# Optimization experiments

Measured on AMD Instinct MI355X. Metric: run time of the kernel, lower is better.

Reference implementation:

```python
import jax, jax.numpy as jnp
import numpy as np

B, S, D, F, H = 64, 1024, 512, 256, 512


def setup_inputs() -> dict:
    key = jax.random.key(0)
    ks = jax.random.split(key, 13)
    sd = lambda fan_in: 1.0 / np.sqrt(fan_in)
    return {
        "x": jax.random.normal(ks[0], (B, D), jnp.float32),
        "encoder_outputs": jax.random.normal(ks[1], (B, S, D), jnp.float32),
        "field_embeddings": jax.random.normal(ks[2], (B, S, F), jnp.float32),
        # Dense params: field_embs_TIL (F->H), enc_outs_TIL (D->H),
        # state_fields_L (D->H), state_enc_outs_L (D->H), out_gate_L (2D->H)
        "W_f": jax.random.normal(ks[3], (F, H), jnp.float32) * sd(F),
        "b_f": jnp.zeros((H,), jnp.float32),
        "W_e": jax.random.normal(ks[4], (D, H), jnp.float32) * sd(D),
        "b_e": jnp.zeros((H,), jnp.float32),
        "W_sf": jax.random.normal(ks[5], (D, H), jnp.float32) * sd(D),
        "b_sf": jnp.zeros((H,), jnp.float32),
        "W_se": jax.random.normal(ks[6], (D, H), jnp.float32) * sd(D),
        "b_se": jnp.zeros((H,), jnp.float32),
        "W_g": jax.random.normal(ks[7], (2 * D, H), jnp.float32) * sd(2 * D),
        "b_g": jnp.zeros((H,), jnp.float32),
    }


def reference(x, encoder_outputs, field_embeddings,
              W_f, b_f, W_e, b_e, W_sf, b_sf, W_se, b_se, W_g, b_g):
    # calc_timestep_consts: seq-major layout [S, B, feat]
    enc_outs = jnp.transpose(encoder_outputs, (1, 0, 2))        # [S,B,D]
    fields = jnp.transpose(field_embeddings, (1, 0, 2))          # [S,B,F]
    fe_TI = jnp.tanh(fields @ W_f + b_f)                         # [S,B,H]
    eo_TI = jnp.tanh(enc_outs @ W_e + b_e)                       # [S,B,H]

    # call(x)
    state_tanh_f = jnp.tanh(x @ W_sf + b_sf)                     # [B,H]
    state_tanh_x = jnp.tanh(x @ W_se + b_se)                     # [B,H]

    score_enc_outs = jnp.einsum('bh,sbh->sb', state_tanh_x, eo_TI)  # [S,B]
    score_fields = jnp.einsum('bh,sbh->sb', state_tanh_f, fe_TI)    # [S,B]
    alphas = jax.nn.softmax(score_enc_outs, axis=0)
    betas = jax.nn.softmax(score_fields, axis=0)

    ab = alphas * betas
    gammas = ab / (1e-6 + jnp.sum(ab, axis=0, keepdims=True))    # [S,B]

    context = jnp.einsum('sb,sbd->bd', gammas, enc_outs)          # [B,D]
    out = jnp.tanh(jnp.concatenate([context, x], axis=-1) @ W_g + b_g)  # [B,H]
    return out, gammas
```

## Files before the change

kernel.cpp:

```cpp
#include <hip/hip_runtime.h>

#define B_ 64
#define S_ 1024
#define D_ 512
#define F_ 256
#define H_ 512

#define FLAGS_W  0
#define ST_F_W   16
#define ST_X_W   32784
#define SC_E_W   65552
#define SC_F_W   131088
#define WPEL_W   196624
#define WPFL_W   327696
#define CTX_W    393232
#define WPEH_W   426000
#define WPFH_W   557072
#define CANARY_W 622608

typedef __attribute__((ext_vector_type(8))) short bf16x8;
typedef __attribute__((ext_vector_type(4))) short bf16x4;
typedef __attribute__((ext_vector_type(4))) float f32x4;
typedef unsigned short u16;
typedef unsigned int u32;

__device__ inline float bf2f(u16 u) {
  u32 i = ((u32)u) << 16;
  float f;
  __builtin_memcpy(&f, &i, 4);
  return f;
}
__device__ inline u16 f2bf(float f) {
  u32 i;
  __builtin_memcpy(&i, &f, 4);
  u32 r = i + 0x7fffu + ((i >> 16) & 1u);
  return (u16)(r >> 16);
}
__device__ inline void split_bf(float v, u16& h, u16& l) {
  u32 i;
  __builtin_memcpy(&i, &v, 4);
  h = (u16)(i >> 16);
  u32 hb = i & 0xFFFF0000u;
  float hf;
  __builtin_memcpy(&hf, &hb, 4);
  l = f2bf(v - hf);
}
__device__ inline u32 cvt_pk_bf16(float a, float b) {
  u32 r;
  asm("v_cvt_pk_bf16_f32 %0, %1, %2" : "=v"(r) : "v"(a), "v"(b));
  return r;
}
__device__ inline float ldin(const void* p, size_t i, int f32) {
  return f32 ? ((const float*)p)[i] : bf2f(((const u16*)p)[i]);
}
__device__ inline void stout(void* p, size_t i, float v, int f32) {
  if (f32) ((float*)p)[i] = v;
  else ((u16*)p)[i] = f2bf(v);
}
__device__ inline float fast_tanh(float x) {
  float cx = fminf(15.f, fmaxf(-15.f, x));
  float e = __expf(2.f * cx);
  return (e - 1.f) * __builtin_amdgcn_rcpf(e + 1.f);
}

__global__ void prep_kernel(const u16* __restrict__ We16,
                            const void* __restrict__ We, const void* __restrict__ Wf,
                            const void* __restrict__ x,
                            const void* __restrict__ Wsf, const void* __restrict__ bsf,
                            const void* __restrict__ Wse, const void* __restrict__ bse,
                            float* __restrict__ st_f, float* __restrict__ st_x,
                            u16* __restrict__ WpEH, u16* __restrict__ WpEL,
                            u16* __restrict__ WpFH, u16* __restrict__ WpFL,
                            u32* __restrict__ flags, u32* __restrict__ canary,
                            float* __restrict__ ctx) {
  __shared__ u32 cnt;
  if (threadIdx.x == 0) cnt = 0;
  __syncthreads();
  u32 local = 0;
  for (int i = threadIdx.x; i < 1024; i += 256) {
    u32 e = (We16[i] >> 7) & 0xFF;
    if (e >= 134) ++local;
  }
  if (local) atomicAdd(&cnt, local);
  __syncthreads();
  const int f32 = cnt > 64;
  const int bid = blockIdx.x, t = threadIdx.x;

  if (bid < 32) {
    int i = bid * 1024 + t * 4;
    *(f32x4*)&ctx[i] = (f32x4){0.f, 0.f, 0.f, 0.f};
    if (bid == 0 && t == 0) {
      flags[0] = (u32)f32;
      for (int i2 = 1; i2 < 16; ++i2) flags[i2] = 0;
      canary[0] = 0xC0DE0001u; canary[1] = 0xC0DE0002u;
      canary[2] = 0xC0DE0003u; canary[3] = 0xC0DE0004u;
    }
    return;
  }
  if (bid < 288) {
    int tid = (bid - 32) * 256 + t;
    int h = tid & 511, b = (tid >> 9) & 63, which = tid >> 15;
    const void* W = which ? Wse : Wsf;
    const void* bias = which ? bse : bsf;
    float a[8] = {};
    for (int d = 0; d < D_; d += 8) {
#pragma unroll
      for (int j = 0; j < 8; ++j)
        a[j] += ldin(x, b * D_ + d + j, f32) * ldin(W, (size_t)(d + j) * H_ + h, f32);
    }
    float acc = ((a[0] + a[1]) + (a[2] + a[3])) + ((a[4] + a[5]) + (a[6] + a[7]));
    float v = fast_tanh(acc + ldin(bias, h, f32));
    (which ? st_x : st_f)[b * H_ + h] = v;
    return;
  }
  int tb = bid - 288;
  const void* W;
  u16 *WpH, *WpL;
  int K;
  if (tb < 128) { W = We; WpH = WpEH; WpL = WpEL; K = 512; }
  else          { W = Wf; WpH = WpFH; WpL = WpFL; K = 256; tb -= 128; }
  int tg = tb * 256 + t;
  int lane = tg & 63, tile = tg >> 6;
  int kc = tile >> 5, nc = tile & 31;
  int kb = kc * 32 + ((lane >> 4) << 3);
  int nb = nc * 16 + (lane & 15);
  u16 vh[8], vl[8];
#pragma unroll
  for (int j = 0; j < 8; ++j) {
    float v = ldin(W, (size_t)(kb + j) * H_ + nb, f32);
    split_bf(v, vh[j], vl[j]);
  }
  size_t off = ((size_t)tile << 9) + (size_t)lane * 8;
#pragma unroll
  for (int j = 0; j < 8; ++j) {
    WpH[off + j] = vh[j];
    WpL[off + j] = vl[j];
  }
}

__global__ void __launch_bounds__(512, 2) score2_kernel(
    const void* __restrict__ enc, const void* __restrict__ fld,
    const u16* __restrict__ WpEH, const u16* __restrict__ WpEL,
    const u16* __restrict__ WpFH, const u16* __restrict__ WpFL,
    const void* __restrict__ be, const void* __restrict__ bfp,
    const float* __restrict__ stx, const float* __restrict__ stf,
    float* __restrict__ sce, float* __restrict__ scf,
    const u32* __restrict__ flags) {
  constexpr int KP = 128, LDK = KP + 8;
  __shared__ __attribute__((aligned(16))) short AsH[2][64 * LDK];
  __shared__ __attribute__((aligned(16))) short AsL[2][64 * LDK];
  __shared__ float scw[8][64];
  const int f32 = flags[0];
  const int tid = threadIdx.x;
  int bid = blockIdx.x;
  const int sel = bid >> 10;
  bid &= 1023;
  const void* A    = sel ? fld : enc;
  const u16* WpH   = sel ? WpFH : WpEH;
  const u16* WpL   = sel ? WpFL : WpEL;
  const void* bias = sel ? bfp : be;
  const float* st  = sel ? stf : stx;
  float* score     = sel ? scf : sce;
  const int K = sel ? F_ : D_;
  const int NPH = K >> 7, NK = NPH * 4;

  const int m0 = bid * 64;
  const int b = m0 >> 10, s0 = m0 & 1023;
  const int lane = tid & 63, wave = tid >> 6;
  const int ml = lane & 15, q = lane >> 4;
  const int nb = wave * 4;
  const bf16x8* wph = (const bf16x8*)WpH;
  const bf16x8* wpl = (const bf16x8*)WpL;
  const int sr = tid >> 5, scc = tid & 31;
  f32x4 pre[4];
  bf16x4 preb[4];

#define ISSUE_LOADS(PH)                                                              \
  do {                                                                               \
    if (f32) {                                                                       \
      _Pragma("unroll") for (int it = 0; it < 4; ++it)                               \
          pre[it] = *(const f32x4*)((const float*)A +                                \
                                    (size_t)(m0 + sr + 16 * it) * K + (PH)*KP + scc * 4); \
    } else {                                                                         \
      _Pragma("unroll") for (int it = 0; it < 4; ++it)                               \
          preb[it] = *(const bf16x4*)((const u16*)A +                                \
                                      (size_t)(m0 + sr + 16 * it) * K + (PH)*KP + scc * 4); \
    }                                                                                \
  } while (0)

#define WRITE_STAGE(BUF)                                                             \
  do {                                                                               \
    _Pragma("unroll") for (int it = 0; it < 4; ++it) {                               \
      u32 iv[4];                                                                     \
      float vf[4];                                                                   \
      if (f32) {                                                                     \
        _Pragma("unroll") for (int j = 0; j < 4; ++j) {                              \
          vf[j] = pre[it][j];                                                        \
          __builtin_memcpy(&iv[j], &vf[j], 4);                                       \
        }                                                                            \
      } else {                                                                       \
        _Pragma("unroll") for (int j = 0; j < 4; ++j) {                              \
          iv[j] = ((u32)(u16)preb[it][j]) << 16;                                     \
          __builtin_memcpy(&vf[j], &iv[j], 4);                                       \
        }                                                                            \
      }                                                                              \
      u32 h01 = __builtin_amdgcn_perm(iv[1], iv[0], 0x07060302u);                    \
      u32 h23 = __builtin_amdgcn_perm(iv[3], iv[2], 0x07060302u);                    \
      float hf[4];                                                                   \
      _Pragma("unroll") for (int j = 0; j < 4; ++j) {                                \
        u32 hb = iv[j] & 0xFFFF0000u;                                                \
        __builtin_memcpy(&hf[j], &hb, 4);                                            \
      }                                                                              \
      u32 l01 = cvt_pk_bf16(vf[0] - hf[0], vf[1] - hf[1]);                           \
      u32 l23 = cvt_pk_bf16(vf[2] - hf[2], vf[3] - hf[3]);                           \
      u32* dH = (u32*)&AsH[BUF][(sr + 16 * it) * LDK + scc * 4];                     \
      u32* dL = (u32*)&AsL[BUF][(sr + 16 * it) * LDK + scc * 4];                     \
      dH[0] = h01; dH[1] = h23;                                                      \
      dL[0] = l01; dL[1] = l23;                                                      \
    }                                                                                \
  } while (0)

#define LOAD_B(DH, DL, KCG)                                                          \
  do {                                                                               \
    _Pragma("unroll") for (int ns = 0; ns < 4; ++ns) {                               \
      size_t widx = (size_t)((KCG)*32 + nb + ns) * 64 + lane;                        \
      DH[ns] = wph[widx];                                                            \
      DL[ns] = wpl[widx];                                                            \
    }                                                                                \
  } while (0)

  f32x4 acc[4][4] = {};
  bf16x8 bh[4], bl[4], bhn[4], bln[4];
  ISSUE_LOADS(0);
  WRITE_STAGE(0);
  ISSUE_LOADS(1);
  LOAD_B(bh, bl, 0);
  __syncthreads();
  for (int ph = 0; ph < NPH; ++ph) {
    const int cur = ph & 1, nxt = cur ^ 1;
#pragma unroll
    for (int kc = 0; kc < 4; ++kc) {
      const int kcg = ph * 4 + kc;
      const int kcn = (kcg + 1 < NK) ? (kcg + 1) : kcg;
      LOAD_B(bhn, bln, kcn);
      bf16x8 ah[4], al[4];
#pragma unroll
      for (int ms = 0; ms < 4; ++ms) {
        ah[ms] = *(const bf16x8*)&AsH[cur][(ms * 16 + ml) * LDK + kc * 32 + q * 8];
        al[ms] = *(const bf16x8*)&AsL[cur][(ms * 16 + ml) * LDK + kc * 32 + q * 8];
      }
      if (kc == 2 && ph + 1 < NPH) WRITE_STAGE(nxt);
      if (kc == 3 && ph + 2 < NPH) ISSUE_LOADS(ph + 2);
      __builtin_amdgcn_s_setprio(1);
#pragma unroll
      for (int ms = 0; ms < 4; ++ms)
#pragma unroll
        for (int ns = 0; ns < 4; ++ns) {
          acc[ms][ns] = __builtin_amdgcn_mfma_f32_16x16x32_bf16(ah[ms], bh[ns], acc[ms][ns], 0, 0, 0);
          acc[ms][ns] = __builtin_amdgcn_mfma_f32_16x16x32_bf16(al[ms], bh[ns], acc[ms][ns], 0, 0, 0);
          acc[ms][ns] = __builtin_amdgcn_mfma_f32_16x16x32_bf16(ah[ms], bl[ns], acc[ms][ns], 0, 0, 0);
        }
      __builtin_amdgcn_s_setprio(0);
#pragma unroll
      for (int ns = 0; ns < 4; ++ns) { bh[ns] = bhn[ns]; bl[ns] = bln[ns]; }
    }
    __syncthreads();
  }
  float biasn[4], stn[4];
#pragma unroll
  for (int ns = 0; ns < 4; ++ns) {
    int n = (nb + ns) * 16 + ml;
    biasn[ns] = ldin(bias, n, f32);
    stn[ns] = st[b * H_ + n];
  }
#pragma unroll
  for (int ms = 0; ms < 4; ++ms) {
#pragma unroll
    for (int r = 0; r < 4; ++r) {
      float p = 0.f;
#pragma unroll
      for (int ns = 0; ns < 4; ++ns)
        p += fast_tanh(acc[ms][ns][r] + biasn[ns]) * stn[ns];
      p += __shfl_xor(p, 1);
      p += __shfl_xor(p, 2);
      p += __shfl_xor(p, 4);
      p += __shfl_xor(p, 8);
      if (ml == 0) scw[wave][ms * 16 + q * 4 + r] = p;
    }
  }
  __syncthreads();
  if (tid < 64) {
    float s = 0.f;
#pragma unroll
    for (int w = 0; w < 8; ++w) s += scw[w][tid];
    score[b * S_ + s0 + tid] = s;
  }
#undef ISSUE_LOADS
#undef WRITE_STAGE
#undef LOAD_B
}

__device__ inline float block_reduce_max(float v, float* red, int tid) {
#pragma unroll
  for (int off = 32; off >= 1; off >>= 1) v = fmaxf(v, __shfl_xor(v, off));
  if ((tid & 63) == 0) red[tid >> 6] = v;
  __syncthreads();
  v = fmaxf(fmaxf(red[0], red[1]), fmaxf(red[2], red[3]));
  __syncthreads();
  return v;
}
__device__ inline float block_reduce_sum(float v, float* red, int tid) {
#pragma unroll
  for (int off = 32; off >= 1; off >>= 1) v += __shfl_xor(v, off);
  if ((tid & 63) == 0) red[tid >> 6] = v;
  __syncthreads();
  v = red[0] + red[1] + red[2] + red[3];
  __syncthreads();
  return v;
}

__global__ void ctx2_kernel(const float* __restrict__ se, const float* __restrict__ sf,
                            const void* __restrict__ enc, float* __restrict__ ctx,
                            void* __restrict__ dout, u32* __restrict__ flags) {
  __shared__ float red[4];
  __shared__ float gl[S_];
  const int f32 = flags[0];
  int b = blockIdx.x >> 4, sc = blockIdx.x & 15;
  int t = threadIdx.x;
  float e[4], f[4];
  int bad = 0;
#pragma unroll
  for (int i = 0; i < 4; ++i) {
    e[i] = se[b * S_ + t + 256 * i];
    f[i] = sf[b * S_ + t + 256 * i];
    if (!(fabsf(e[i]) < 1e4f) || !(fabsf(f[i]) < 1e4f)) bad = 1;
  }
  if (bad && sc == 0) flags[4] = 1;
  float me = block_reduce_max(fmaxf(fmaxf(e[0], e[1]), fmaxf(e[2], e[3])), red, t);
  float mf = block_reduce_max(fmaxf(fmaxf(f[0], f[1]), fmaxf(f[2], f[3])), red, t);
  float sume = 0.f, sumf = 0.f;
#pragma unroll
  for (int i = 0; i < 4; ++i) {
    e[i] = __expf(e[i] - me);
    sume += e[i];
    f[i] = __expf(f[i] - mf);
    sumf += f[i];
  }
  sume = block_reduce_sum(sume, red, t);
  sumf = block_reduce_sum(sumf, red, t);
  float g[4], tot = 0.f;
#pragma unroll
  for (int i = 0; i < 4; ++i) {
    g[i] = (e[i] / sume) * (f[i] / sumf);
    tot += g[i];
  }
  tot = block_reduce_sum(tot, red, t);
  float scale = 1.f / (1e-6f + tot);
#pragma unroll
  for (int i = 0; i < 4; ++i) {
    int s = t + 256 * i;
    float gv = g[i] * scale;
    gl[s] = gv;
    if (sc == 0) stout(dout, (size_t)B_ * H_ + (size_t)s * B_ + b, gv, f32);
  }
  __syncthreads();
  int d0 = t * 2;
  float a0 = 0.f, a1 = 0.f;
#pragma unroll 4
  for (int s = sc * 64; s < sc * 64 + 64; ++s) {
    float gv = gl[s];
    size_t base = ((size_t)(b * S_ + s)) * D_ + d0;
    a0 += gv * ldin(enc, base, f32);
    a1 += gv * ldin(enc, base + 1, f32);
  }
  atomicAdd(&ctx[b * D_ + d0], a0);
  atomicAdd(&ctx[b * D_ + d0 + 1], a1);
}

__global__ void out_kernel(const float* __restrict__ ctx, const void* __restrict__ x,
                           const void* __restrict__ Wg, const void* __restrict__ bg,
                           void* __restrict__ dout, const u32* __restrict__ flags,
                           const u32* __restrict__ canary) {
  const int f32 = flags[0];
  int tid = blockIdx.x * 256 + threadIdx.x;
  int h = tid & 511, b = tid >> 9;
  float a0 = 0.f, a1 = 0.f, a2 = 0.f, a3 = 0.f;
  for (int d = 0; d < D_; d += 4) {
    a0 += ctx[b * D_ + d]     * ldin(Wg, (size_t)d * H_ + h, f32);
    a1 += ctx[b * D_ + d + 1] * ldin(Wg, (size_t)(d + 1) * H_ + h, f32);
    a2 += ctx[b * D_ + d + 2] * ldin(Wg, (size_t)(d + 2) * H_ + h, f32);
    a3 += ctx[b * D_ + d + 3] * ldin(Wg, (size_t)(d + 3) * H_ + h, f32);
  }
  for (int d = 0; d < D_; d += 4) {
    a0 += ldin(x, b * D_ + d, f32)     * ldin(Wg, (size_t)(D_ + d) * H_ + h, f32);
    a1 += ldin(x, b * D_ + d + 1, f32) * ldin(Wg, (size_t)(D_ + d + 1) * H_ + h, f32);
    a2 += ldin(x, b * D_ + d + 2, f32) * ldin(Wg, (size_t)(D_ + d + 2) * H_ + h, f32);
    a3 += ldin(x, b * D_ + d + 3, f32) * ldin(Wg, (size_t)(D_ + d + 3) * H_ + h, f32);
  }
  float acc = (a0 + a1) + (a2 + a3);
  float v = fast_tanh(acc + ldin(bg, h, f32));
  if (tid == 0) {
    u32 code = 0;
    if (canary[0] != 0xC0DE0001u || canary[1] != 0xC0DE0002u ||
        canary[2] != 0xC0DE0003u || canary[3] != 0xC0DE0004u) code += 32;
    if (flags[4]) code += 64;
    if (code) v = (float)code;
  }
  stout(dout, (size_t)b * H_ + h, v, f32);
}

extern "C" void kernel_launch(void* const* d_in, const int* in_sizes, int n_in,
                              void* d_out, int out_size, void* d_ws, size_t ws_size,
                              hipStream_t stream) {
  const void* x    = d_in[0];
  const void* enc  = d_in[1];
  const void* fld  = d_in[2];
  const void* W_f  = d_in[3];
  const void* b_f  = d_in[4];
  const void* W_e  = d_in[5];
  const void* b_e  = d_in[6];
  const void* W_sf = d_in[7];
  const void* b_sf = d_in[8];
  const void* W_se = d_in[9];
  const void* b_se = d_in[10];
  const void* W_g  = d_in[11];
  const void* b_g  = d_in[12];

  float* ws    = (float*)d_ws;
  u32* flags   = (u32*)(ws + FLAGS_W);
  float* st_f  = ws + ST_F_W;
  float* st_x  = ws + ST_X_W;
  float* sc_e  = ws + SC_E_W;
  float* sc_f  = ws + SC_F_W;
  float* ctx   = ws + CTX_W;
  u16* WpEH    = (u16*)(ws + WPEH_W);
  u16* WpEL    = (u16*)(ws + WPEL_W);
  u16* WpFH    = (u16*)(ws + WPFH_W);
  u16* WpFL    = (u16*)(ws + WPFL_W);
  u32* canary  = (u32*)(ws + CANARY_W);

  prep_kernel<<<480, 256, 0, stream>>>((const u16*)W_e, W_e, W_f, x,
                                       W_sf, b_sf, W_se, b_se, st_f, st_x,
                                       WpEH, WpEL, WpFH, WpFL, flags, canary, ctx);
  score2_kernel<<<2048, 512, 0, stream>>>(enc, fld, WpEH, WpEL, WpFH, WpFL,
                                          b_e, b_f, st_x, st_f, sc_e, sc_f, flags);
  ctx2_kernel<<<1024, 256, 0, stream>>>(sc_e, sc_f, enc, ctx, d_out, flags);
  out_kernel<<<128, 256, 0, stream>>>(ctx, x, W_g, b_g, d_out, flags, canary);
}
```

Measured before the change: 560.7 us.

## Specialize score kernel on K and hoist dtype branches out of inner loops

Turns the score GEMM body into a template on K so the phase loop fully unrolls, and precomputes byte offsets for LDS and B-fragment addressing. It also double-buffers the B fragments by index instead of copying registers each step. In the prep, context and output kernels, the per-element ldin dtype switch is replaced by separate f32 and bf16 loops using pointer-increment addressing. The intent is less address arithmetic and branching in hot loops, at the cost of larger code and more register pressure.

```diff
diff --git a/kernel.cpp b/kernel.cpp
--- a/kernel.cpp
+++ b/kernel.cpp
@@ -21,6 +21,7 @@
 typedef __attribute__((ext_vector_type(8))) short bf16x8;
 typedef __attribute__((ext_vector_type(4))) short bf16x4;
 typedef __attribute__((ext_vector_type(4))) float f32x4;
+typedef __attribute__((ext_vector_type(2))) unsigned int u32x2;
 typedef unsigned short u16;
 typedef unsigned int u32;
 
@@ -100,15 +101,24 @@
   if (bid < 288) {
     int tid = (bid - 32) * 256 + t;
     int h = tid & 511, b = (tid >> 9) & 63, which = tid >> 15;
-    const void* W = which ? Wse : Wsf;
+    float a[8] = {};
+    if (f32) {
+      const float* xp = (const float*)x + b * D_;
+      const float* Wp = (const float*)(which ? Wse : Wsf) + h;
+      for (int d = 0; d < D_; d += 8)
+#pragma unroll
+        for (int j = 0; j < 8; ++j)
+          a[j] += xp[d + j] * Wp[(size_t)(d + j) * H_];
+    } else {
+      const u16* xp = (const u16*)x + b * D_;
+      const u16* Wp = (const u16*)(which ? Wse : Wsf) + h;
+      for (int d = 0; d < D_; d += 8)
+#pragma unroll
+        for (int j = 0; j < 8; ++j)
+          a[j] += bf2f(xp[d + j]) * bf2f(Wp[(size_t)(d + j) * H_]);
+    }
+    float acc = ((a[0] + a[1]) + (a[2] + a[3])) + ((a[4] + a[5]) + (a[6] + a[7]));
     const void* bias = which ? bse : bsf;
-    float a[8] = {};
-    for (int d = 0; d < D_; d += 8) {
-#pragma unroll
-      for (int j = 0; j < 8; ++j)
-        a[j] += ldin(x, b * D_ + d + j, f32) * ldin(W, (size_t)(d + j) * H_ + h, f32);
-    }
-    float acc = ((a[0] + a[1]) + (a[2] + a[3])) + ((a[4] + a[5]) + (a[6] + a[7]));
     float v = fast_tanh(acc + ldin(bias, h, f32));
     (which ? st_x : st_f)[b * H_ + h] = v;
     return;
@@ -116,20 +126,26 @@
   int tb = bid - 288;
   const void* W;
   u16 *WpH, *WpL;
-  int K;
-  if (tb < 128) { W = We; WpH = WpEH; WpL = WpEL; K = 512; }
-  else          { W = Wf; WpH = WpFH; WpL = WpFL; K = 256; tb -= 128; }
+  if (tb < 128) { W = We; WpH = WpEH; WpL = WpEL; }
+  else          { W = Wf; WpH = WpFH; WpL = WpFL; tb -= 128; }
   int tg = tb * 256 + t;
   int lane = tg & 63, tile = tg >> 6;
   int kc = tile >> 5, nc = tile & 31;
   int kb = kc * 32 + ((lane >> 4) << 3);
   int nb = nc * 16 + (lane & 15);
+  float v[8];
+  if (f32) {
+    const float* Wp = (const float*)W + (size_t)kb * H_ + nb;
+#pragma unroll
+    for (int j = 0; j < 8; ++j) v[j] = Wp[(size_t)j * H_];
+  } else {
+    const u16* Wp = (const u16*)W + (size_t)kb * H_ + nb;
+#pragma unroll
+    for (int j = 0; j < 8; ++j) v[j] = bf2f(Wp[(size_t)j * H_]);
+  }
   u16 vh[8], vl[8];
 #pragma unroll
-  for (int j = 0; j < 8; ++j) {
-    float v = ldin(W, (size_t)(kb + j) * H_ + nb, f32);
-    split_bf(v, vh[j], vl[j]);
-  }
+  for (int j = 0; j < 8; ++j) split_bf(v[j], vh[j], vl[j]);
   size_t off = ((size_t)tile << 9) + (size_t)lane * 8;
 #pragma unroll
   for (int j = 0; j < 8; ++j) {
@@ -138,40 +154,24 @@
   }
 }
 
-__global__ void __launch_bounds__(512, 2) score2_kernel(
-    const void* __restrict__ enc, const void* __restrict__ fld,
-    const u16* __restrict__ WpEH, const u16* __restrict__ WpEL,
-    const u16* __restrict__ WpFH, const u16* __restrict__ WpFL,
-    const void* __restrict__ be, const void* __restrict__ bfp,
-    const float* __restrict__ stx, const float* __restrict__ stf,
-    float* __restrict__ sce, float* __restrict__ scf,
-    const u32* __restrict__ flags) {
-  constexpr int KP = 128, LDK = KP + 8;
-  __shared__ __attribute__((aligned(16))) short AsH[2][64 * LDK];
-  __shared__ __attribute__((aligned(16))) short AsL[2][64 * LDK];
-  __shared__ float scw[8][64];
-  const int f32 = flags[0];
-  const int tid = threadIdx.x;
-  int bid = blockIdx.x;
-  const int sel = bid >> 10;
-  bid &= 1023;
-  const void* A    = sel ? fld : enc;
-  const u16* WpH   = sel ? WpFH : WpEH;
-  const u16* WpL   = sel ? WpFL : WpEL;
-  const void* bias = sel ? bfp : be;
-  const float* st  = sel ? stf : stx;
-  float* score     = sel ? scf : sce;
-  const int K = sel ? F_ : D_;
-  const int NPH = K >> 7, NK = NPH * 4;
+template <int K>
+__device__ __forceinline__ void score_core(
+    const void* __restrict__ A, const bf16x8* __restrict__ wph,
+    const bf16x8* __restrict__ wpl, const void* __restrict__ bias,
+    const float* __restrict__ st, float* __restrict__ score,
+    int f32, int bid, int tid, char* AsHb, char* AsLb, float (*scw)[64]) {
+  constexpr int KP = 128, LDK = KP + 8, NPH = K / KP, NK = NPH * 4;
+  constexpr int BUFB = 64 * LDK * 2;
 
   const int m0 = bid * 64;
   const int b = m0 >> 10, s0 = m0 & 1023;
   const int lane = tid & 63, wave = tid >> 6;
   const int ml = lane & 15, q = lane >> 4;
   const int nb = wave * 4;
-  const bf16x8* wph = (const bf16x8*)WpH;
-  const bf16x8* wpl = (const bf16x8*)WpL;
   const int sr = tid >> 5, scc = tid & 31;
+  const u32 bofsB = ((u32)(nb * 64 + lane)) * 16u;
+  const u32 aoffB = ((u32)(ml * LDK + q * 8)) * 2u;
+  const u32 woffB = ((u32)(sr * LDK + scc * 4)) * 2u;
   f32x4 pre[4];
   bf16x4 preb[4];
 
@@ -211,58 +211,58 @@
         u32 hb = iv[j] & 0xFFFF0000u;                                                \
         __builtin_memcpy(&hf[j], &hb, 4);                                            \
       }                                                                              \
-      u32 l01 = cvt_pk_bf16(vf[0] - hf[0], vf[1] - hf[1]);                           \
-      u32 l23 = cvt_pk_bf16(vf[2] - hf[2], vf[3] - hf[3]);                           \
-      u32* dH = (u32*)&AsH[BUF][(sr + 16 * it) * LDK + scc * 4];                     \
-      u32* dL = (u32*)&AsL[BUF][(sr + 16 * it) * LDK + scc * 4];                     \
-      dH[0] = h01; dH[1] = h23;                                                      \
-      dL[0] = l01; dL[1] = l23;                                                      \
+      u32x2 hv = {h01, h23};                                                         \
+      u32x2 lv = {cvt_pk_bf16(vf[0] - hf[0], vf[1] - hf[1]),                         \
+                  cvt_pk_bf16(vf[2] - hf[2], vf[3] - hf[3])};                        \
+      *(u32x2*)(AsHb + (BUF)*BUFB + it * 4352 + woffB) = hv;                         \
+      *(u32x2*)(AsLb + (BUF)*BUFB + it * 4352 + woffB) = lv;                         \
     }                                                                                \
   } while (0)
 
-#define LOAD_B(DH, DL, KCG)                                                          \
+#define LOAD_B(P, KCG)                                                               \
   do {                                                                               \
+    const char* hp_ = (const char*)(wph + (size_t)(KCG)*2048) + bofsB;               \
+    const char* lp_ = (const char*)(wpl + (size_t)(KCG)*2048) + bofsB;               \
     _Pragma("unroll") for (int ns = 0; ns < 4; ++ns) {                               \
-      size_t widx = (size_t)((KCG)*32 + nb + ns) * 64 + lane;                        \
-      DH[ns] = wph[widx];                                                            \
-      DL[ns] = wpl[widx];                                                            \
+      bhp[P][ns] = *(const bf16x8*)(hp_ + ns * 1024);                                \
+      blp[P][ns] = *(const bf16x8*)(lp_ + ns * 1024);                                \
     }                                                                                \
   } while (0)
 
   f32x4 acc[4][4] = {};
-  bf16x8 bh[4], bl[4], bhn[4], bln[4];
+  bf16x8 bhp[2][4], blp[2][4];
   ISSUE_LOADS(0);
   WRITE_STAGE(0);
   ISSUE_LOADS(1);
-  LOAD_B(bh, bl, 0);
-  __syncthreads();
+  LOAD_B(0, 0);
+  __syncthreads();
+#pragma unroll
   for (int ph = 0; ph < NPH; ++ph) {
-    const int cur = ph & 1, nxt = cur ^ 1;
+    const int cur = ph & 1;
 #pragma unroll
     for (int kc = 0; kc < 4; ++kc) {
       const int kcg = ph * 4 + kc;
+      const int use = kcg & 1, nxp = use ^ 1;
       const int kcn = (kcg + 1 < NK) ? (kcg + 1) : kcg;
-      LOAD_B(bhn, bln, kcn);
+      LOAD_B(nxp, kcn);
       bf16x8 ah[4], al[4];
 #pragma unroll
       for (int ms = 0; ms < 4; ++ms) {
-        ah[ms] = *(const bf16x8*)&AsH[cur][(ms * 16 + ml) * LDK + kc * 32 + q * 8];
-        al[ms] = *(const bf16x8*)&AsL[cur][(ms * 16 + ml) * LDK + kc * 32 + q * 8];
+        ah[ms] = *(const bf16x8*)(AsHb + cur * BUFB + ms * 4352 + kc * 64 + aoffB);
+        al[ms] = *(const bf16x8*)(AsLb + cur * BUFB + ms * 4352 + kc * 64 + aoffB);
       }
-      if (kc == 2 && ph + 1 < NPH) WRITE_STAGE(nxt);
+      if (kc == 2 && ph + 1 < NPH) WRITE_STAGE(cur ^ 1);
       if (kc == 3 && ph + 2 < NPH) ISSUE_LOADS(ph + 2);
       __builtin_amdgcn_s_setprio(1);
 #pragma unroll
       for (int ms = 0; ms < 4; ++ms)
 #pragma unroll
         for (int ns = 0; ns < 4; ++ns) {
-          acc[ms][ns] = __builtin_amdgcn_mfma_f32_16x16x32_bf16(ah[ms], bh[ns], acc[ms][ns], 0, 0, 0);
-          acc[ms][ns] = __builtin_amdgcn_mfma_f32_16x16x32_bf16(al[ms], bh[ns], acc[ms][ns], 0, 0, 0);
-          acc[ms][ns] = __builtin_amdgcn_mfma_f32_16x16x32_bf16(ah[ms], bl[ns], acc[ms][ns], 0, 0, 0);
+          acc[ms][ns] = __builtin_amdgcn_mfma_f32_16x16x32_bf16(ah[ms], bhp[use][ns], acc[ms][ns], 0, 0, 0);
+          acc[ms][ns] = __builtin_amdgcn_mfma_f32_16x16x32_bf16(al[ms], bhp[use][ns], acc[ms][ns], 0, 0, 0);
+          acc[ms][ns] = __builtin_amdgcn_mfma_f32_16x16x32_bf16(ah[ms], blp[use][ns], acc[ms][ns], 0, 0, 0);
         }
       __builtin_amdgcn_s_setprio(0);
-#pragma unroll
-      for (int ns = 0; ns < 4; ++ns) { bh[ns] = bhn[ns]; bl[ns] = bln[ns]; }
     }
     __syncthreads();
   }
@@ -298,6 +298,30 @@
 #undef ISSUE_LOADS
 #undef WRITE_STAGE
 #undef LOAD_B
+}
+
+__global__ void __launch_bounds__(512, 2) score2_kernel(
+    const void* __restrict__ enc, const void* __restrict__ fld,
+    const u16* __restrict__ WpEH, const u16* __restrict__ WpEL,
+    const u16* __restrict__ WpFH, const u16* __restrict__ WpFL,
+    const void* __restrict__ be, const void* __restrict__ bfp,
+    const float* __restrict__ stx, const float* __restrict__ stf,
+    float* __restrict__ sce, float* __restrict__ scf,
+    const u32* __restrict__ flags) {
+  constexpr int LDK = 136;
+  __shared__ __attribute__((aligned(16))) short AsH[2][64 * LDK];
+  __shared__ __attribute__((aligned(16))) short AsL[2][64 * LDK];
+  __shared__ float scw[8][64];
+  const int f32 = flags[0];
+  const int tid = threadIdx.x;
+  int bid = blockIdx.x;
+  if (bid < 1024) {
+    score_core<512>(enc, (const bf16x8*)WpEH, (const bf16x8*)WpEL, be, stx, sce,
+                    f32, bid, tid, (char*)AsH, (char*)AsL, scw);
+  } else {
+    score_core<256>(fld, (const bf16x8*)WpFH, (const bf16x8*)WpFL, bfp, stf, scf,
+                    f32, bid - 1024, tid, (char*)AsH, (char*)AsL, scw);
+  }
 }
 
 __device__ inline float block_reduce_max(float v, float* red, int tid) {
@@ -366,12 +390,26 @@
   __syncthreads();
   int d0 = t * 2;
   float a0 = 0.f, a1 = 0.f;
+  if (f32) {
+    const float* ep = (const float*)enc + ((size_t)(b * S_ + sc * 64)) * D_ + d0;
+    const float* glp = &gl[sc * 64];
 #pragma unroll 4
-  for (int s = sc * 64; s < sc * 64 + 64; ++s) {
-    float gv = gl[s];
-    size_t base = ((size_t)(b * S_ + s)) * D_ + d0;
-    a0 += gv * ldin(enc, base, f32);
-    a1 += gv * ldin(enc, base + 1, f32);
+    for (int s = 0; s < 64; ++s) {
+      float gv = glp[s];
+      a0 += gv * ep[0];
+      a1 += gv * ep[1];
+      ep += D_;
+    }
+  } else {
+    const u16* ep = (const u16*)enc + ((size_t)(b * S_ + sc * 64)) * D_ + d0;
+    const float* glp = &gl[sc * 64];
+#pragma unroll 4
+    for (int s = 0; s < 64; ++s) {
+      float gv = glp[s];
+      a0 += gv * bf2f(ep[0]);
+      a1 += gv * bf2f(ep[1]);
+      ep += D_;
+    }
   }
   atomicAdd(&ctx[b * D_ + d0], a0);
   atomicAdd(&ctx[b * D_ + d0 + 1], a1);
@@ -384,18 +422,40 @@
   const int f32 = flags[0];
   int tid = blockIdx.x * 256 + threadIdx.x;
   int h = tid & 511, b = tid >> 9;
+  const float* cp = ctx + b * D_;
   float a0 = 0.f, a1 = 0.f, a2 = 0.f, a3 = 0.f;
-  for (int d = 0; d < D_; d += 4) {
-    a0 += ctx[b * D_ + d]     * ldin(Wg, (size_t)d * H_ + h, f32);
-    a1 += ctx[b * D_ + d + 1] * ldin(Wg, (size_t)(d + 1) * H_ + h, f32);
-    a2 += ctx[b * D_ + d + 2] * ldin(Wg, (size_t)(d + 2) * H_ + h, f32);
-    a3 += ctx[b * D_ + d + 3] * ldin(Wg, (size_t)(d + 3) * H_ + h, f32);
-  }
-  for (int d = 0; d < D_; d += 4) {
-    a0 += ldin(x, b * D_ + d, f32)     * ldin(Wg, (size_t)(D_ + d) * H_ + h, f32);
-    a1 += ldin(x, b * D_ + d + 1, f32) * ldin(Wg, (size_t)(D_ + d + 1) * H_ + h, f32);
-    a2 += ldin(x, b * D_ + d + 2, f32) * ldin(Wg, (size_t)(D_ + d + 2) * H_ + h, f32);
-    a3 += ldin(x, b * D_ + d + 3, f32) * ldin(Wg, (size_t)(D_ + d + 3) * H_ + h, f32);
+  if (f32) {
+    const float* Wgp = (const float*)Wg + h;
+    const float* xp = (const float*)x + b * D_;
+    for (int d = 0; d < D_; d += 4) {
+      a0 += cp[d]     * Wgp[(size_t)d * H_];
+      a1 += cp[d + 1] * Wgp[(size_t)(d + 1) * H_];
+      a2 += cp[d + 2] * Wgp[(size_t)(d + 2) * H_];
+      a3 += cp[d + 3] * Wgp[(size_t)(d + 3) * H_];
+    }
+    const float* Wgx = Wgp + (size_t)D_ * H_;
+    for (int d = 0; d < D_; d += 4) {
+      a0 += xp[d]     * Wgx[(size_t)d * H_];
+      a1 += xp[d + 1] * Wgx[(size_t)(d + 1) * H_];
+      a2 += xp[d + 2] * Wgx[(size_t)(d + 2) * H_];
+      a3 += xp[d + 3] * Wgx[(size_t)(d + 3) * H_];
+    }
+  } else {
+    const u16* Wgp = (const u16*)Wg + h;
+    const u16* xp = (const u16*)x + b * D_;
+    for (int d = 0; d < D_; d += 4) {
+      a0 += cp[d]     * bf2f(Wgp[(size_t)d * H_]);
+      a1 += cp[d + 1] * bf2f(Wgp[(size_t)(d + 1) * H_]);
+      a2 += cp[d + 2] * bf2f(Wgp[(size_t)(d + 2) * H_]);
+      a3 += cp[d + 3] * bf2f(Wgp[(size_t)(d + 3) * H_]);
+    }
+    const u16* Wgx = Wgp + (size_t)D_ * H_;
+    for (int d = 0; d < D_; d += 4) {
+      a0 += bf2f(xp[d])     * bf2f(Wgx[(size_t)d * H_]);
+      a1 += bf2f(xp[d + 1]) * bf2f(Wgx[(size_t)(d + 1) * H_]);
+      a2 += bf2f(xp[d + 2]) * bf2f(Wgx[(size_t)(d + 2) * H_]);
+      a3 += bf2f(xp[d + 3]) * bf2f(Wgx[(size_t)(d + 3) * H_]);
+    }
   }
   float acc = (a0 + a1) + (a2 + a3);
   float v = fast_tanh(acc + ldin(bg, h, f32));
```

Result: faster. 455.3 us (-18.8%).
